# Optimization experiments

Hardware: AMD Instinct MI355X
Metric: run time of the kernel (lower is better)

Reference implementation:

```python
import jax, jax.numpy as jnp
import numpy as np

jax.config.update("jax_enable_x64", True)

# --- static config (matches init_kwargs) ---
L = 6            # voxel_level_num
F = 8            # feature_dim
T = 524288       # per-level feature table size
B = 4194304      # buffer_size (hash table size)
N = 1048576      # number of query points
LEAF = 0.25      # leaf_voxel_size
UP = 2.0         # up_scale_factor

PRIMES = jnp.array([73856093, 19349669, 83492791], dtype=jnp.int64)
# corner offsets, z varies fastest (same order as torch self.steps)
STEPS = jnp.array([[0,0,0],[0,0,1],[0,1,0],[0,1,1],
                   [1,0,0],[1,0,1],[1,1,0],[1,1,1]], dtype=jnp.float32)


def setup_inputs() -> dict:
    key = jax.random.key(0)
    k1, k2, k3, k4 = jax.random.split(key, 4)
    query_points = jax.random.uniform(k1, (N, 3), dtype=jnp.float32) * 50.0
    features = 0.01 * jax.random.normal(k2, (L, T, F), dtype=jnp.float32)
    idx = jax.random.randint(k3, (L, B), 0, T, dtype=jnp.int64)
    empty = jax.random.uniform(k4, (L, B)) < 0.2
    feature_indexs = jnp.where(empty, jnp.int64(-1), idx)
    return {"query_points": query_points, "features": features,
            "feature_indexs": feature_indexs}


def _trilinear_coeffs(d):
    # d: [N,3] fractional coords in the cell; order matches STEPS (z fastest)
    tx, ty, tz = d[:, 0], d[:, 1], d[:, 2]
    return jnp.stack([
        (1-tx)*(1-ty)*(1-tz), (1-tx)*(1-ty)*tz,
        (1-tx)*ty*(1-tz),     (1-tx)*ty*tz,
        tx*(1-ty)*(1-tz),     tx*(1-ty)*tz,
        tx*ty*(1-tz),         tx*ty*tz,
    ], axis=1)  # [N,8]


def reference(query_points, features, feature_indexs):
    out = jnp.zeros((query_points.shape[0], F), dtype=query_points.dtype)
    for i in range(L):  # small fixed level loop (structurally distinct resolutions)
        res = LEAF * (UP ** i)
        scaled = query_points / res                      # [N,3]
        base = jnp.floor(scaled)
        corners = (base[:, None, :] + STEPS[None]).astype(jnp.int64)  # [N,8,3]
        keys = jnp.mod((corners * PRIMES).sum(-1), B)    # [N,8] spatial hash
        idx = feature_indexs[i][keys]                    # [N,8] gather, -1 = empty
        valid = idx.min(axis=1) > -1                     # [N] all 8 corners allocated
        coeffs = _trilinear_coeffs(scaled - base)        # [N,8]
        feats = features[i][jnp.clip(idx, 0, T - 1)]     # [N,8,F] gather
        level = jnp.einsum('nkf,nk->nf', feats, coeffs)  # trilinear interp
        out = out + jnp.where(valid[:, None], level, jnp.zeros((), out.dtype))
    return out
```

## Files before the change

### kernel.cpp

```cpp
#include <hip/hip_runtime.h>


static constexpr int      NPTS  = 1048576;
static constexpr int      NF    = 8;
static constexpr int      TTAB  = 524288;
static constexpr unsigned BTAB  = 4194304u;
static constexpr unsigned BMASK = BTAB - 1u;
static constexpr unsigned P0 = 73856093u, P1 = 19349669u, P2 = 83492791u;

static constexpr int NBIN = 4096;
static constexpr int SB   = 256;
static constexpr int PPB  = NPTS / SB;
static constexpr int ITER = PPB / 256;
static constexpr int BCAP = 512;

static constexpr int S2 = 51, S3 = 26, S4 = 14, S5 = 8;
static constexpr int OCC2 = 0, OCC3 = OCC2 + S2*S2, OCC4 = OCC3 + S3*S3,
                     OCC5 = OCC4 + S4*S4, OCCW = OCC5 + S5*S5;
static constexpr int CB2 = 0, CB3 = CB2 + (S2-1)*(S2-1),
                     CB4 = CB3 + (S3-1)*(S3-1), CB5 = CB4 + (S4-1)*(S4-1),
                     CBW = CB5 + (S5-1)*(S5-1);
static constexpr int RB2 = (S2*S2+3)/4, RB3 = (S3*S3+3)/4,
                     RB4 = (S4*S4+3)/4, RB5 = (S5*S5+3)/4;
static constexpr int OCCB = RB2+RB3+RB4+RB5;

static constexpr int L0S = 201, L0C = 200, L0W = 4;
static constexpr int L1S = 101, L1C = 100, L1W = 2;
static constexpr int L0R = L0S * L0S;
static constexpr int L1R = L1S * L1S;
static constexpr int OCC0W_CNT = L0R * L0W;
static constexpr int OCC1W_CNT = L1R * L1W;
static constexpr int CB0_CNT = L0C * L0C * L0W;
static constexpr int CB1_CNT = L1C * L1C * L1W;
static constexpr int OCC01_WAVES = OCC0W_CNT + OCC1W_CNT;
static constexpr int OCC01_B = (OCC01_WAVES + 3) / 4;
static constexpr int MIDC = CBW + CB0_CNT + CB1_CNT;
static constexpr int MIDB = 16 + (MIDC + 255) / 256;

static constexpr int BM01_WAVES = (int)(2 * BTAB / 256);
static constexpr int BM01B = BM01_WAVES / 4;

static constexpr size_t HIST_OFF      = 0;
static constexpr size_t OUT_BM01_OFF  = 4u  * 1024 * 1024;
static constexpr size_t OUT_OCC25_OFF = 5u  * 1024 * 1024;
static constexpr size_t OUT_OCC0_OFF  = 5632u * 1024;
static constexpr size_t OUT_OCC1_OFF  = 7u  * 1024 * 1024;

static constexpr size_t SORTED_BYTES = (size_t)NPTS * 16;
static constexpr size_t CB25_OFF = SORTED_BYTES;
static constexpr size_t CB0_OFF  = CB25_OFF + 32768;
static constexpr size_t CB1_OFF  = CB0_OFF + 1310720;
static constexpr size_t BB_OFF   = CB1_OFF + 163840;
static constexpr size_t WS_FULL  = BB_OFF + (size_t)NBIN * 4;

typedef float f4 __attribute__((ext_vector_type(4)));
typedef int   i4 __attribute__((ext_vector_type(4)));

__device__ __forceinline__ void nhv_point_g(
    float qx, float qy, float qz,
    const float* __restrict__ feat, const int* __restrict__ fidx,
    const unsigned long long* __restrict__ cbit25,
    const unsigned long long* __restrict__ cbit0,
    const unsigned long long* __restrict__ cbit1, float acc[NF])
{
    const int ix0 = (int)(qx * 4.0f), iy0 = (int)(qy * 4.0f), iz0 = (int)(qz * 4.0f);
    const int ix1 = (int)(qx * 2.0f), iy1 = (int)(qy * 2.0f), iz1 = (int)(qz * 2.0f);

    const unsigned long long w0 = cbit0[(size_t)(iz0 * L0C + iy0) * L0W + (ix0 >> 6)];
    const unsigned long long w1 = cbit1[(size_t)(iz1 * L1C + iy1) * L1W + (ix1 >> 6)];

    float fxh[4], fyh[4], fzh[4];
    int   ixh[4], iyh[4], izh[4];
    unsigned vm = 0;
    vm |= (unsigned)((w0 >> (ix0 & 63)) & 1ull) << 0;
    vm |= (unsigned)((w1 >> (ix1 & 63)) & 1ull) << 1;
    const int Ss[4]  = {S2, S3, S4, S5};
    const int CBo[4] = {CB2, CB3, CB4, CB5};
#pragma unroll
    for (int j = 0; j < 4; ++j) {
        const float inv = 1.0f / (float)(1 << j);
        const float sx = qx*inv, sy = qy*inv, sz = qz*inv;
        const float bx = floorf(sx), by = floorf(sy), bz = floorf(sz);
        fxh[j] = sx-bx; fyh[j] = sy-by; fzh[j] = sz-bz;
        ixh[j] = (int)bx; iyh[j] = (int)by; izh[j] = (int)bz;
        const int C = Ss[j] - 1;
        const unsigned long long row = cbit25[CBo[j] + izh[j]*C + iyh[j]];
        vm |= (unsigned)((row >> ixh[j]) & 1ull) << (2 + j);
    }

#pragma unroll
    for (int f = 0; f < NF; ++f) acc[f] = 0.0f;

#pragma unroll
    for (int i = 0; i < 2; ++i) {
        if (vm & (1u << i)) {
            const float inv = (i == 0) ? 4.0f : 2.0f;
            const float sx = qx*inv, sy = qy*inv, sz = qz*inv;
            const float bx = floorf(sx), by = floorf(sy), bz = floorf(sz);
            const unsigned h = (unsigned)(int)bx*P0 + (unsigned)(int)by*P1
                             + (unsigned)(int)bz*P2;
            const int* __restrict__ tab = fidx + (size_t)i * BTAB;
            int id[8];
#pragma unroll
            for (int k = 0; k < 8; ++k) {
                unsigned key = h;
                if (k & 4) key += P0;
                if (k & 2) key += P1;
                if (k & 1) key += P2;
                id[k] = tab[key & BMASK];
            }
            const float tx = sx - bx, ty = sy - by, tz = sz - bz;
            const float wxv[2] = {1.0f - tx, tx};
            const float wyv[2] = {1.0f - ty, ty};
            const float wzv[2] = {1.0f - tz, tz};
            const float* __restrict__ fb = feat + (size_t)i * (TTAB * NF);
#pragma unroll
            for (int k = 0; k < 8; ++k) {
                const float c = wxv[(k>>2)&1] * wyv[(k>>1)&1] * wzv[k&1];
                const float4* p = (const float4*)(fb + (size_t)id[k] * NF);
                const float4 lo = p[0], hi = p[1];
                acc[0]+=c*lo.x; acc[1]+=c*lo.y; acc[2]+=c*lo.z; acc[3]+=c*lo.w;
                acc[4]+=c*hi.x; acc[5]+=c*hi.y; acc[6]+=c*hi.z; acc[7]+=c*hi.w;
            }
        }
    }
#pragma unroll
    for (int j = 0; j < 4; ++j) {
        if (vm & (1u << (2 + j))) {
            const int lvl = 2 + j;
            const unsigned h = (unsigned)ixh[j]*P0 + (unsigned)iyh[j]*P1
                             + (unsigned)izh[j]*P2;
            const int* __restrict__ tab = fidx + (size_t)lvl * BTAB;
            int id[8];
#pragma unroll
            for (int k = 0; k < 8; ++k) {
                unsigned key = h;
                if (k & 4) key += P0;
                if (k & 2) key += P1;
                if (k & 1) key += P2;
                id[k] = tab[key & BMASK];
            }
            const float wxv[2] = {1.0f - fxh[j], fxh[j]};
            const float wyv[2] = {1.0f - fyh[j], fyh[j]};
            const float wzv[2] = {1.0f - fzh[j], fzh[j]};
            const float* __restrict__ fb = feat + (size_t)lvl * (TTAB * NF);
#pragma unroll
            for (int k = 0; k < 8; ++k) {
                const float c = wxv[(k>>2)&1] * wyv[(k>>1)&1] * wzv[k&1];
                const float4* p = (const float4*)(fb + (size_t)id[k] * NF);
                const float4 lo = p[0], hi = p[1];
                acc[0]+=c*lo.x; acc[1]+=c*lo.y; acc[2]+=c*lo.z; acc[3]+=c*lo.w;
                acc[4]+=c*hi.x; acc[5]+=c*hi.y; acc[6]+=c*hi.z; acc[7]+=c*hi.w;
            }
        }
    }
}

__device__ __forceinline__ void nhv_point(
    float qx, float qy, float qz,
    const float* __restrict__ feat, const int* __restrict__ fidx, float acc[NF])
{
    float fx[6], fy[6], fz[6];
    unsigned h[6];
#pragma unroll
    for (int i = 0; i < 6; ++i) {
        const float inv = 4.0f / (float)(1 << i);
        const float sx = qx*inv, sy = qy*inv, sz = qz*inv;
        const float bx = floorf(sx), by = floorf(sy), bz = floorf(sz);
        fx[i] = sx-bx; fy[i] = sy-by; fz[i] = sz-bz;
        h[i] = (unsigned)(int)bx*P0 + (unsigned)(int)by*P1 + (unsigned)(int)bz*P2;
    }
    int id[6][8];
#pragma unroll
    for (int i = 0; i < 6; ++i) {
        const int* __restrict__ tab = fidx + (size_t)i * BTAB;
#pragma unroll
        for (int k = 0; k < 8; ++k) {
            unsigned key = h[i];
            if (k & 4) key += P0;
            if (k & 2) key += P1;
            if (k & 1) key += P2;
            id[i][k] = tab[key & BMASK];
        }
    }
#pragma unroll
    for (int f = 0; f < NF; ++f) acc[f] = 0.0f;
#pragma unroll
    for (int i = 0; i < 6; ++i) {
        int mn = id[i][0];
#pragma unroll
        for (int k = 1; k < 8; ++k) mn = min(mn, id[i][k]);
        if (mn > -1) {
            const float wxv[2] = {1.0f - fx[i], fx[i]};
            const float wyv[2] = {1.0f - fy[i], fy[i]};
            const float wzv[2] = {1.0f - fz[i], fz[i]};
            const float* __restrict__ fb = feat + (size_t)i * (TTAB * NF);
#pragma unroll
            for (int k = 0; k < 8; ++k) {
                const float c = wxv[(k>>2)&1] * wyv[(k>>1)&1] * wzv[k&1];
                const float4* p = (const float4*)(fb + (size_t)id[i][k] * NF);
                const float4 lo = p[0], hi = p[1];
                acc[0]+=c*lo.x; acc[1]+=c*lo.y; acc[2]+=c*lo.z; acc[3]+=c*lo.w;
                acc[4]+=c*hi.x; acc[5]+=c*hi.y; acc[6]+=c*hi.z; acc[7]+=c*hi.w;
            }
        }
    }
}

__device__ __forceinline__ unsigned expand4(unsigned v) {
    return (v & 1u) | ((v & 2u) << 2) | ((v & 4u) << 4) | ((v & 8u) << 6);
}
__device__ __forceinline__ unsigned bin_of(float x, float y, float z) {
    unsigned bx = min(15u, (unsigned)(int)(x * 0.32f));
    unsigned by = min(15u, (unsigned)(int)(y * 0.32f));
    unsigned bz = min(15u, (unsigned)(int)(z * 0.32f));
    return expand4(bx) | (expand4(by) << 1) | (expand4(bz) << 2);
}

__global__ __launch_bounds__(256) void pre_k(const int* __restrict__ fidx,
                                             unsigned long long* __restrict__ occ25,
                                             unsigned long long* __restrict__ bm01,
                                             const float* __restrict__ qp,
                                             unsigned* __restrict__ hist) {
    __shared__ unsigned lh[NBIN];
    const int t = threadIdx.x, b = blockIdx.x;
    if (b < OCCB) {
        int lvl, S, occoff, bb = b;
        if (bb < RB2)              { lvl = 2; S = S2; occoff = OCC2; }
        else if ((bb -= RB2) < RB3){ lvl = 3; S = S3; occoff = OCC3; }
        else if ((bb -= RB3) < RB4){ lvl = 4; S = S4; occoff = OCC4; }
        else        { bb -= RB4;     lvl = 5; S = S5; occoff = OCC5; }
        const int row  = bb * 4 + (t >> 6);
        const int lane = t & 63;
        if (row < S * S) {
            const int y = row % S, z = row / S;
            bool v = false;
            if (lane < S) {
                const unsigned key = ((unsigned)lane*P0 + (unsigned)y*P1
                                    + (unsigned)z*P2) & BMASK;
                v = fidx[(size_t)lvl * BTAB + key] >= 0;
            }
            const unsigned long long m = __ballot(v);
            if (lane == 0) occ25[occoff + row] = m;
        }
    } else if (b < OCCB + BM01B) {
        const int tid  = (b - OCCB) * 256 + t;
        const int w    = tid >> 6;
        const int lane = tid & 63;
        const i4 v = __builtin_nontemporal_load(
                        (const i4*)(fidx + (size_t)w * 256) + lane);
        const unsigned long long m0 = __ballot(v.x >= 0);
        const unsigned long long m1 = __ballot(v.y >= 0);
        const unsigned long long m2 = __ballot(v.z >= 0);
        const unsigned long long m3 = __ballot(v.w >= 0);
        if (lane == 0) {
            unsigned long long* d = bm01 + ((size_t)w << 2);
            d[0] = m0; d[1] = m1; d[2] = m2; d[3] = m3;
        }
    } else {
        const int bh = b - OCCB - BM01B;
        for (int i = t; i < NBIN; i += 256) lh[i] = 0u;
        __syncthreads();
        const int base = bh * PPB;
#pragma unroll
        for (int i = 0; i < ITER; ++i) {
            const int p = base + i * 256 + t;
            const float x = __builtin_nontemporal_load(qp + 3*p);
            const float y = __builtin_nontemporal_load(qp + 3*p + 1);
            const float z = __builtin_nontemporal_load(qp + 3*p + 2);
            atomicAdd(&lh[bin_of(x, y, z)], 1u);
        }
        __syncthreads();
        for (int i = t; i < NBIN; i += 256)
            __builtin_nontemporal_store(lh[i], hist + (size_t)bh * NBIN + i);
    }
}

__global__ __launch_bounds__(256) void occ01_k(
    const unsigned long long* __restrict__ bm01,
    unsigned long long* __restrict__ occ0,
    unsigned long long* __restrict__ occ1)
{
    const int wid  = (blockIdx.x * 256 + threadIdx.x) >> 6;
    const int lane = threadIdx.x & 63;
    if (wid >= OCC01_WAVES) return;

    int lvl, S, row, wblk;
    unsigned long long* dst;
    if (wid < OCC0W_CNT) {
        lvl = 0; S = L0S; row = wid >> 2; wblk = wid & 3; dst = occ0 + wid;
    } else {
        const int w1 = wid - OCC0W_CNT;
        lvl = 1; S = L1S; row = w1 >> 1; wblk = w1 & 1; dst = occ1 + w1;
    }
    const int z = row / S, y = row % S;
    const int x = wblk * 64 + lane;
    bool v = false;
    if (x < S) {
        const unsigned key = ((unsigned)x*P0 + (unsigned)y*P1 + (unsigned)z*P2) & BMASK;
        const unsigned B = (unsigned)lvl * BTAB + key;
        const unsigned long long word = bm01[((size_t)(B >> 8) << 2) | (B & 3u)];
        v = (word >> ((B >> 2) & 63u)) & 1ull;
    }
    const unsigned long long m = __ballot(v);
    if (lane == 0) *dst = m;
}

__global__ __launch_bounds__(256) void mid_k(unsigned* __restrict__ hist,
                                             unsigned* __restrict__ binbase,
                                             const unsigned long long* __restrict__ occ25,
                                             const unsigned long long* __restrict__ occ0,
                                             const unsigned long long* __restrict__ occ1,
                                             unsigned long long* __restrict__ cbit25,
                                             unsigned long long* __restrict__ cbit0,
                                             unsigned long long* __restrict__ cbit1) {
    const int t = threadIdx.x, b = blockIdx.x;
    if (b < 16) {
        const int bin = b * 256 + t;
        unsigned run = 0;
        for (int blk = 0; blk < SB; ++blk) {
            const unsigned v = hist[(size_t)blk * NBIN + bin];
            hist[(size_t)blk * NBIN + bin] = run;
            run += v;
        }
        binbase[bin] = run;
        return;
    }
    const int c = (b - 16) * 256 + t;
    if (c >= MIDC) return;
    if (c < CBW) {
        int S, occoff, cboff, local;
        if (c < CB3)      { S = S2; occoff = OCC2; cboff = CB2; local = c; }
        else if (c < CB4) { S = S3; occoff = OCC3; cboff = CB3; local = c - CB3; }
        else if (c < CB5) { S = S4; occoff = OCC4; cboff = CB4; local = c - CB4; }
        else              { S = S5; occoff = OCC5; cboff = CB5; local = c - CB5; }
        const int C = S - 1;
        const int cy = local % C, cz = local / C;
        const unsigned long long r00 = occ25[occoff +  cz      * S + cy    ];
        const unsigned long long r10 = occ25[occoff +  cz      * S + cy + 1];
        const unsigned long long r01 = occ25[occoff + (cz + 1) * S + cy    ];
        const unsigned long long r11 = occ25[occoff + (cz + 1) * S + cy + 1];
        cbit25[cboff + cz * C + cy] = (r00 & (r00 >> 1)) & (r10 & (r10 >> 1))
                                    & (r01 & (r01 >> 1)) & (r11 & (r11 >> 1));
    } else if (c < CBW + CB0_CNT) {
        const int c0 = c - CBW;
        const int w = c0 & 3, crow = c0 >> 2;
        const int cy = crow % L0C, cz = crow / L0C;
        unsigned long long res = ~0ull;
#pragma unroll
        for (int dy = 0; dy < 2; ++dy)
#pragma unroll
            for (int dz = 0; dz < 2; ++dz) {
                const unsigned long long* r =
                    occ0 + ((size_t)((cz + dz) * L0S + (cy + dy)) << 2);
                const unsigned long long a = r[w];
                const unsigned long long n = (w < 3) ? r[w + 1] : 0ull;
                res &= a & ((a >> 1) | (n << 63));
            }
        cbit0[c0] = res;
    } else {
        const int c1 = c - CBW - CB0_CNT;
        const int w = c1 & 1, crow = c1 >> 1;
        const int cy = crow % L1C, cz = crow / L1C;
        unsigned long long res = ~0ull;
#pragma unroll
        for (int dy = 0; dy < 2; ++dy)
#pragma unroll
            for (int dz = 0; dz < 2; ++dz) {
                const unsigned long long* r =
                    occ1 + ((size_t)((cz + dz) * L1S + (cy + dy)) << 1);
                const unsigned long long a = r[w];
                const unsigned long long n = (w < 1) ? r[w + 1] : 0ull;
                res &= a & ((a >> 1) | (n << 63));
            }
        cbit1[c1] = res;
    }
}

__global__ __launch_bounds__(256) void binscan_k(unsigned* __restrict__ binbase) {
    __shared__ unsigned tot[256];
    const int t = threadIdx.x;
    unsigned v[16];
    unsigned s = 0;
#pragma unroll
    for (int i = 0; i < 16; ++i) { v[i] = s; s += binbase[t * 16 + i]; }
    tot[t] = s;
    __syncthreads();
    for (int d = 1; d < 256; d <<= 1) {
        const unsigned x = (t >= d) ? tot[t - d] : 0u;
        __syncthreads();
        tot[t] += x;
        __syncthreads();
    }
    const unsigned cb = tot[t] - s;
#pragma unroll
    for (int i = 0; i < 16; ++i) binbase[t * 16 + i] = cb + v[i];
}

__global__ __launch_bounds__(256) void scatter_k(const float* __restrict__ qp,
                                                 const unsigned* __restrict__ hist,
                                                 const unsigned* __restrict__ binbase,
                                                 float4* __restrict__ sorted) {
    __shared__ unsigned cur[NBIN];
    const int b = blockIdx.x, t = threadIdx.x;
    for (int i = t; i < NBIN; i += 256)
        cur[i] = binbase[i] + hist[(size_t)b * NBIN + i];
    __syncthreads();
    const int base = b * PPB;
#pragma unroll
    for (int i = 0; i < ITER; ++i) {
        const int p = base + i * 256 + t;
        const float x = __builtin_nontemporal_load(qp + 3*p);
        const float y = __builtin_nontemporal_load(qp + 3*p + 1);
        const float z = __builtin_nontemporal_load(qp + 3*p + 2);
        const unsigned slot = atomicAdd(&cur[bin_of(x, y, z)], 1u);
        const f4 v = {x, y, z, __uint_as_float((unsigned)p)};
        __builtin_nontemporal_store(v, (f4*)sorted + slot);
    }
}

__global__ __launch_bounds__(256) void binsort_k(float4* __restrict__ sorted,
                                                 const unsigned* __restrict__ binbase) {
    __shared__ float4        pts[BCAP];
    __shared__ unsigned char sk[BCAP];
    __shared__ unsigned      cnt[64];
    const int bin = blockIdx.x, t = threadIdx.x;
    const unsigned start = binbase[bin];
    const unsigned end   = (bin < NBIN - 1) ? binbase[bin + 1] : (unsigned)NPTS;
    const int n = (int)(end - start);
    if (n <= 1 || n > BCAP) return;

    if (t < 64) cnt[t] = 0u;
    __syncthreads();
#pragma unroll
    for (int r = 0; r < BCAP / 256; ++r) {
        const int i = r * 256 + t;
        if (i < n) {
            const f4 pv = __builtin_nontemporal_load((const f4*)sorted + (start + i));
            const float4 p = make_float4(pv.x, pv.y, pv.z, pv.w);
            pts[i] = p;
            const unsigned ux = (unsigned)(int)(p.x * 1.28f) & 3u;
            const unsigned uy = (unsigned)(int)(p.y * 1.28f) & 3u;
            const unsigned uz = (unsigned)(int)(p.z * 1.28f) & 3u;
            const unsigned s = (ux & 1u) | ((uy & 1u) << 1) | ((uz & 1u) << 2)
                             | ((ux >> 1) << 3) | ((uy >> 1) << 4) | ((uz >> 1) << 5);
            sk[i] = (unsigned char)s;
            atomicAdd(&cnt[s], 1u);
        }
    }
    __syncthreads();
    if (t == 0) {
        unsigned run = 0;
#pragma unroll
        for (int i = 0; i < 64; ++i) { const unsigned v = cnt[i]; cnt[i] = run; run += v; }
    }
    __syncthreads();
#pragma unroll
    for (int r = 0; r < BCAP / 256; ++r) {
        const int i = r * 256 + t;
        if (i < n) {
            const unsigned dest = atomicAdd(&cnt[sk[i]], 1u);
            const float4 p = pts[i];
            const f4 v = {p.x, p.y, p.z, p.w};
            __builtin_nontemporal_store(v, (f4*)sorted + (start + dest));
        }
    }
}

__global__ __launch_bounds__(256) void nhv_main_k(
    const float4* __restrict__ sp, const float* __restrict__ feat,
    const int* __restrict__ fidx,
    const unsigned long long* __restrict__ cbit25,
    const unsigned long long* __restrict__ cbit0,
    const unsigned long long* __restrict__ cbit1,
    float* __restrict__ out)
{
    const int nwg = NPTS / 256;
    const int bid = blockIdx.x;
    const int swz = (bid & 7) * (nwg >> 3) + (bid >> 3);
    const int j   = swz * 256 + (int)threadIdx.x;

    const f4 s = __builtin_nontemporal_load((const f4*)sp + j);
    float acc[NF];
    nhv_point_g(s.x, s.y, s.z, feat, fidx, cbit25, cbit0, cbit1, acc);
    const unsigned n = __float_as_uint(s.w);
    f4* o = (f4*)(out + (size_t)n * NF);
    f4 lo = {acc[0], acc[1], acc[2], acc[3]};
    f4 hi = {acc[4], acc[5], acc[6], acc[7]};
    __builtin_nontemporal_store(lo, o);
    __builtin_nontemporal_store(hi, o + 1);
}

__global__ __launch_bounds__(256) void nhv_direct_k(
    const float* __restrict__ qp, const float* __restrict__ feat,
    const int* __restrict__ fidx, float* __restrict__ out)
{
    const int n = blockIdx.x * 256 + threadIdx.x;
    if (n >= NPTS) return;
    float acc[NF];
    nhv_point(qp[3*n], qp[3*n+1], qp[3*n+2], feat, fidx, acc);
    float4* o = (float4*)(out + (size_t)n * NF);
    o[0] = make_float4(acc[0], acc[1], acc[2], acc[3]);
    o[1] = make_float4(acc[4], acc[5], acc[6], acc[7]);
}

extern "C" void kernel_launch(void* const* d_in, const int* in_sizes, int n_in,
                              void* d_out, int out_size, void* d_ws, size_t ws_size,
                              hipStream_t stream) {
    const float* qp   = (const float*)d_in[0];
    const float* feat = (const float*)d_in[1];
    const int*   fidx = (const int*)d_in[2];
    float*       out  = (float*)d_out;

    if (ws_size >= WS_FULL) {
        float4*             sorted  = (float4*)d_ws;
        unsigned long long* cbit25  = (unsigned long long*)((char*)d_ws + CB25_OFF);
        unsigned long long* cbit0   = (unsigned long long*)((char*)d_ws + CB0_OFF);
        unsigned long long* cbit1   = (unsigned long long*)((char*)d_ws + CB1_OFF);
        unsigned*           binbase = (unsigned*)((char*)d_ws + BB_OFF);
        unsigned*           hist  = (unsigned*)d_out;
        unsigned long long* bm01  = (unsigned long long*)((char*)d_out + OUT_BM01_OFF);
        unsigned long long* occ25 = (unsigned long long*)((char*)d_out + OUT_OCC25_OFF);
        unsigned long long* occ0  = (unsigned long long*)((char*)d_out + OUT_OCC0_OFF);
        unsigned long long* occ1  = (unsigned long long*)((char*)d_out + OUT_OCC1_OFF);

        pre_k<<<dim3(OCCB + BM01B + SB), dim3(256), 0, stream>>>(fidx, occ25, bm01, qp, hist);
        occ01_k<<<dim3(OCC01_B), dim3(256), 0, stream>>>(bm01, occ0, occ1);
        mid_k<<<dim3(MIDB), dim3(256), 0, stream>>>(hist, binbase, occ25, occ0, occ1,
                                                    cbit25, cbit0, cbit1);
        binscan_k<<<dim3(1), dim3(256), 0, stream>>>(binbase);
        scatter_k<<<dim3(SB), dim3(256), 0, stream>>>(qp, hist, binbase, sorted);
        binsort_k<<<dim3(NBIN), dim3(256), 0, stream>>>(sorted, binbase);
        nhv_main_k<<<dim3(NPTS/256), dim3(256), 0, stream>>>(sorted, feat, fidx,
                                                             cbit25, cbit0, cbit1, out);
    } else {
        nhv_direct_k<<<dim3(NPTS/256), dim3(256), 0, stream>>>(qp, feat, fidx, out);
    }
}
```

Measured before the change: 215.1 us.

## Fold level-0/1 occupancy gather into pre_k and process two points per thread

Removes the intermediate bitmap pass over feature_indexs for levels 0 and 1, which streamed 32MB. Occupancy words are now computed by direct hashed gathers inside pre_k, and the separate occ01_k launch is dropped. The main interpolation kernel also handles two sorted points per thread with half the blocks, which exposes more independent gathers per thread at the cost of higher register pressure.

Measured after the change: 319.6 us. 1.49x slower.

```diff
diff --git a/kernel.cpp b/kernel.cpp
--- a/kernel.cpp
+++ b/kernel.cpp
@@ -26,25 +26,18 @@
 
 static constexpr int L0S = 201, L0C = 200, L0W = 4;
 static constexpr int L1S = 101, L1C = 100, L1W = 2;
-static constexpr int L0R = L0S * L0S;
-static constexpr int L1R = L1S * L1S;
-static constexpr int OCC0W_CNT = L0R * L0W;
-static constexpr int OCC1W_CNT = L1R * L1W;
+static constexpr int OCC0W_CNT = L0S * L0S * L0W;
+static constexpr int OCC1W_CNT = L1S * L1S * L1W;
 static constexpr int CB0_CNT = L0C * L0C * L0W;
 static constexpr int CB1_CNT = L1C * L1C * L1W;
 static constexpr int OCC01_WAVES = OCC0W_CNT + OCC1W_CNT;
-static constexpr int OCC01_B = (OCC01_WAVES + 3) / 4;
+static constexpr int V01B = (OCC01_WAVES + 3) / 4;
 static constexpr int MIDC = CBW + CB0_CNT + CB1_CNT;
 static constexpr int MIDB = 16 + (MIDC + 255) / 256;
 
-static constexpr int BM01_WAVES = (int)(2 * BTAB / 256);
-static constexpr int BM01B = BM01_WAVES / 4;
-
-static constexpr size_t HIST_OFF      = 0;
-static constexpr size_t OUT_BM01_OFF  = 4u  * 1024 * 1024;
-static constexpr size_t OUT_OCC25_OFF = 5u  * 1024 * 1024;
-static constexpr size_t OUT_OCC0_OFF  = 5632u * 1024;
-static constexpr size_t OUT_OCC1_OFF  = 7u  * 1024 * 1024;
+static constexpr size_t OUT_OCC25_OFF = 4u * 1024 * 1024;
+static constexpr size_t OUT_OCC0_OFF  = OUT_OCC25_OFF + 262144;
+static constexpr size_t OUT_OCC1_OFF  = OUT_OCC0_OFF + 1572864;
 
 static constexpr size_t SORTED_BYTES = (size_t)NPTS * 16;
 static constexpr size_t CB25_OFF = SORTED_BYTES;
@@ -54,7 +47,6 @@
 static constexpr size_t WS_FULL  = BB_OFF + (size_t)NBIN * 4;
 
 typedef float f4 __attribute__((ext_vector_type(4)));
-typedef int   i4 __attribute__((ext_vector_type(4)));
 
 __device__ __forceinline__ void nhv_point_g(
     float qx, float qy, float qz,
@@ -219,7 +211,8 @@
 
 __global__ __launch_bounds__(256) void pre_k(const int* __restrict__ fidx,
                                              unsigned long long* __restrict__ occ25,
-                                             unsigned long long* __restrict__ bm01,
+                                             unsigned long long* __restrict__ occ0,
+                                             unsigned long long* __restrict__ occ1,
                                              const float* __restrict__ qp,
                                              unsigned* __restrict__ hist) {
     __shared__ unsigned lh[NBIN];
@@ -243,22 +236,34 @@
             const unsigned long long m = __ballot(v);
             if (lane == 0) occ25[occoff + row] = m;
         }
-    } else if (b < OCCB + BM01B) {
-        const int tid  = (b - OCCB) * 256 + t;
-        const int w    = tid >> 6;
-        const int lane = tid & 63;
-        const i4 v = __builtin_nontemporal_load(
-                        (const i4*)(fidx + (size_t)w * 256) + lane);
-        const unsigned long long m0 = __ballot(v.x >= 0);
-        const unsigned long long m1 = __ballot(v.y >= 0);
-        const unsigned long long m2 = __ballot(v.z >= 0);
-        const unsigned long long m3 = __ballot(v.w >= 0);
-        if (lane == 0) {
-            unsigned long long* d = bm01 + ((size_t)w << 2);
-            d[0] = m0; d[1] = m1; d[2] = m2; d[3] = m3;
+    } else if (b < OCCB + V01B) {
+        const int wid  = (b - OCCB) * 4 + (t >> 6);
+        const int lane = t & 63;
+        if (wid < OCC01_WAVES) {
+            int S, row, wblk;
+            const int* __restrict__ tab;
+            unsigned long long* dst;
+            if (wid < OCC0W_CNT) {
+                S = L0S; row = wid >> 2; wblk = wid & 3;
+                tab = fidx;        dst = occ0 + wid;
+            } else {
+                const int w1 = wid - OCC0W_CNT;
+                S = L1S; row = w1 >> 1; wblk = w1 & 1;
+                tab = fidx + BTAB; dst = occ1 + w1;
+            }
+            const int z = row / S, y = row % S;
+            const int x = wblk * 64 + lane;
+            bool v = false;
+            if (x < S) {
+                const unsigned key = ((unsigned)x*P0 + (unsigned)y*P1
+                                    + (unsigned)z*P2) & BMASK;
+                v = tab[key] >= 0;
+            }
+            const unsigned long long m = __ballot(v);
+            if (lane == 0) *dst = m;
         }
     } else {
-        const int bh = b - OCCB - BM01B;
+        const int bh = b - OCCB - V01B;
         for (int i = t; i < NBIN; i += 256) lh[i] = 0u;
         __syncthreads();
         const int base = bh * PPB;
@@ -274,36 +279,6 @@
         for (int i = t; i < NBIN; i += 256)
             __builtin_nontemporal_store(lh[i], hist + (size_t)bh * NBIN + i);
     }
-}
-
-__global__ __launch_bounds__(256) void occ01_k(
-    const unsigned long long* __restrict__ bm01,
-    unsigned long long* __restrict__ occ0,
-    unsigned long long* __restrict__ occ1)
-{
-    const int wid  = (blockIdx.x * 256 + threadIdx.x) >> 6;
-    const int lane = threadIdx.x & 63;
-    if (wid >= OCC01_WAVES) return;
-
-    int lvl, S, row, wblk;
-    unsigned long long* dst;
-    if (wid < OCC0W_CNT) {
-        lvl = 0; S = L0S; row = wid >> 2; wblk = wid & 3; dst = occ0 + wid;
-    } else {
-        const int w1 = wid - OCC0W_CNT;
-        lvl = 1; S = L1S; row = w1 >> 1; wblk = w1 & 1; dst = occ1 + w1;
-    }
-    const int z = row / S, y = row % S;
-    const int x = wblk * 64 + lane;
-    bool v = false;
-    if (x < S) {
-        const unsigned key = ((unsigned)x*P0 + (unsigned)y*P1 + (unsigned)z*P2) & BMASK;
-        const unsigned B = (unsigned)lvl * BTAB + key;
-        const unsigned long long word = bm01[((size_t)(B >> 8) << 2) | (B & 3u)];
-        v = (word >> ((B >> 2) & 63u)) & 1ull;
-    }
-    const unsigned long long m = __ballot(v);
-    if (lane == 0) *dst = m;
 }
 
 __global__ __launch_bounds__(256) void mid_k(unsigned* __restrict__ hist,
@@ -475,20 +450,31 @@
     const unsigned long long* __restrict__ cbit1,
     float* __restrict__ out)
 {
-    const int nwg = NPTS / 256;
+    const int nwg = NPTS / 512;
     const int bid = blockIdx.x;
     const int swz = (bid & 7) * (nwg >> 3) + (bid >> 3);
-    const int j   = swz * 256 + (int)threadIdx.x;
-
-    const f4 s = __builtin_nontemporal_load((const f4*)sp + j);
-    float acc[NF];
-    nhv_point_g(s.x, s.y, s.z, feat, fidx, cbit25, cbit0, cbit1, acc);
-    const unsigned n = __float_as_uint(s.w);
-    f4* o = (f4*)(out + (size_t)n * NF);
-    f4 lo = {acc[0], acc[1], acc[2], acc[3]};
-    f4 hi = {acc[4], acc[5], acc[6], acc[7]};
-    __builtin_nontemporal_store(lo, o);
-    __builtin_nontemporal_store(hi, o + 1);
+    const int j0  = swz * 512 + (int)threadIdx.x;
+    const int j1  = j0 + 256;
+
+    const f4 s0 = __builtin_nontemporal_load((const f4*)sp + j0);
+    const f4 s1 = __builtin_nontemporal_load((const f4*)sp + j1);
+
+    float a0[NF], a1[NF];
+    nhv_point_g(s0.x, s0.y, s0.z, feat, fidx, cbit25, cbit0, cbit1, a0);
+    nhv_point_g(s1.x, s1.y, s1.z, feat, fidx, cbit25, cbit0, cbit1, a1);
+
+    const unsigned n0 = __float_as_uint(s0.w);
+    const unsigned n1 = __float_as_uint(s1.w);
+    f4* o0 = (f4*)(out + (size_t)n0 * NF);
+    f4* o1 = (f4*)(out + (size_t)n1 * NF);
+    f4 l0 = {a0[0], a0[1], a0[2], a0[3]};
+    f4 h0 = {a0[4], a0[5], a0[6], a0[7]};
+    f4 l1 = {a1[0], a1[1], a1[2], a1[3]};
+    f4 h1 = {a1[4], a1[5], a1[6], a1[7]};
+    __builtin_nontemporal_store(l0, o0);
+    __builtin_nontemporal_store(h0, o0 + 1);
+    __builtin_nontemporal_store(l1, o1);
+    __builtin_nontemporal_store(h1, o1 + 1);
 }
 
 __global__ __launch_bounds__(256) void nhv_direct_k(
@@ -519,19 +505,17 @@
         unsigned long long* cbit1   = (unsigned long long*)((char*)d_ws + CB1_OFF);
         unsigned*           binbase = (unsigned*)((char*)d_ws + BB_OFF);
         unsigned*           hist  = (unsigned*)d_out;
-        unsigned long long* bm01  = (unsigned long long*)((char*)d_out + OUT_BM01_OFF);
         unsigned long long* occ25 = (unsigned long long*)((char*)d_out + OUT_OCC25_OFF);
         unsigned long long* occ0  = (unsigned long long*)((char*)d_out + OUT_OCC0_OFF);
         unsigned long long* occ1  = (unsigned long long*)((char*)d_out + OUT_OCC1_OFF);
 
-        pre_k<<<dim3(OCCB + BM01B + SB), dim3(256), 0, stream>>>(fidx, occ25, bm01, qp, hist);
-        occ01_k<<<dim3(OCC01_B), dim3(256), 0, stream>>>(bm01, occ0, occ1);
+        pre_k<<<dim3(OCCB + V01B + SB), dim3(256), 0, stream>>>(fidx, occ25, occ0, occ1, qp, hist);
         mid_k<<<dim3(MIDB), dim3(256), 0, stream>>>(hist, binbase, occ25, occ0, occ1,
                                                     cbit25, cbit0, cbit1);
         binscan_k<<<dim3(1), dim3(256), 0, stream>>>(binbase);
         scatter_k<<<dim3(SB), dim3(256), 0, stream>>>(qp, hist, binbase, sorted);
         binsort_k<<<dim3(NBIN), dim3(256), 0, stream>>>(sorted, binbase);
-        nhv_main_k<<<dim3(NPTS/256), dim3(256), 0, stream>>>(sorted, feat, fidx,
+        nhv_main_k<<<dim3(NPTS/512), dim3(256), 0, stream>>>(sorted, feat, fidx,
                                                              cbit25, cbit0, cbit1, out);
     } else {
         nhv_direct_k<<<dim3(NPTS/256), dim3(256), 0, stream>>>(qp, feat, fidx, out);
```
